# Kernel tuning notes

Hardware: AMD Instinct MI355X
Metric: run time of the kernel (lower is better)

The kernel has to match this reference:

```python
import jax, jax.numpy as jnp
import numpy as np

B, T, C = 4, 4096, 1024
HEAD_SIZE = 64
HEAD_OUT = 64


def setup_inputs() -> dict:
    key = jax.random.key(0)
    kx, kk, kq, kv = jax.random.split(key, 4)
    x = jax.random.normal(kx, (B, T, C), dtype=jnp.float32)
    # nn.Linear(in, out, bias=False): weight [out, in]; y = x @ W.T
    Wk = jax.random.normal(kk, (HEAD_SIZE, C), dtype=jnp.float32) * (C ** -0.5)
    Wq = jax.random.normal(kq, (HEAD_SIZE, C), dtype=jnp.float32) * (C ** -0.5)
    Wv = jax.random.normal(kv, (HEAD_OUT, C), dtype=jnp.float32) * (C ** -0.5)
    return {"x": x, "Wk": Wk, "Wq": Wq, "Wv": Wv}


def reference(x, Wk, Wq, Wv):
    Tlen = x.shape[1]
    k = jnp.einsum('btc,hc->bth', x, Wk)  # [B,T,Hs]
    q = jnp.einsum('btc,hc->bth', x, Wq)  # [B,T,Hs]
    v = jnp.einsum('btc,oc->bto', x, Wv)  # [B,T,Ho]
    scale = HEAD_SIZE ** -0.5
    scores = jnp.einsum('bih,bjh->bij', q, k) * scale  # [B,T,T]
    # torch.tril(ones, diagonal=1): allowed where j <= i+1 (note: one superdiagonal kept)
    i = jnp.arange(Tlen)[:, None]
    j = jnp.arange(Tlen)[None, :]
    allowed = j <= i + 1
    masked = jnp.where(allowed, scores, -jnp.inf)
    # NOTE: original scales AGAIN inside softmax (double scaling, faithful)
    weights = jax.nn.softmax(masked * scale, axis=-1)
    return jnp.einsum('bij,bjo->bio', weights, v)  # [B,T,Ho]
```

## Files before the change

### kernel.cpp

```cpp
#include <hip/hip_runtime.h>

#define BB 4
#define TT 4096
#define CC 1024
#define HH 64
#define AW 8

typedef unsigned short us;
typedef us v8u __attribute__((ext_vector_type(8)));
typedef us v4u __attribute__((ext_vector_type(4)));
typedef __bf16 v8bf __attribute__((ext_vector_type(8)));
typedef float v4f __attribute__((ext_vector_type(4)));

__device__ __forceinline__ us f2bf(float f) {
  return __builtin_bit_cast(us, (__bf16)f);
}
__device__ __forceinline__ v8bf ldb(const us* p) {
  return __builtin_bit_cast(v8bf, *(const v8u*)p);
}

__global__ __launch_bounds__(256) void convertw_kernel(const float* __restrict__ Wk,
                                                       const float* __restrict__ Wq,
                                                       const float* __restrict__ Wv,
                                                       us* __restrict__ wpack) {
  const int g = blockIdx.x * 256 + threadIdx.x;
  const int t = g >> 13;
  const int rem = g & 8191;
  const int oc = rem >> 11;
  const int kc = (rem >> 6) & 31;
  const int lane = rem & 63;
  const float* W = (t == 0) ? Wq : ((t == 1) ? Wk : Wv);
  const int h  = oc * 16 + (lane & 15);
  const int d0 = kc * 32 + (lane >> 4) * 8;
  const float4* src = (const float4*)(W + h * CC + d0);
  const float4 f0 = src[0], f1 = src[1];
  v8u o;
  o[0]=f2bf(f0.x); o[1]=f2bf(f0.y); o[2]=f2bf(f0.z); o[3]=f2bf(f0.w);
  o[4]=f2bf(f1.x); o[5]=f2bf(f1.y); o[6]=f2bf(f1.z); o[7]=f2bf(f1.w);
  *(v8u*)(wpack + (size_t)g * 8) = o;
}


__global__ __launch_bounds__(768, 6) void proj_kernel(
    const float* __restrict__ x, const us* __restrict__ wpack,
    us* __restrict__ qpack, us* __restrict__ kpack, us* __restrict__ vpack)
{
  __shared__ __align__(16) us xlds[32][1048];

  const int tid  = threadIdx.x;
  const int lane = tid & 63, w = tid >> 6;
  const int i16 = lane & 15, quad = lane >> 4;
  const int t = w >> 2, oc = w & 3;
  const int rows0 = blockIdx.x * 32;

  const float4* xg4 = (const float4*)(x + (size_t)rows0 * CC);
  for (int i = tid; i < 8192; i += 768) {
    const float4 f = xg4[i];
    v4u o; o[0]=f2bf(f.x); o[1]=f2bf(f.y); o[2]=f2bf(f.z); o[3]=f2bf(f.w);
    *(v4u*)&xlds[i >> 8][(i & 255) * 4] = o;
  }
  __syncthreads();

  const us* wp = wpack + (size_t)w * 16384 + lane * 8;
  v4f zero = {0.f, 0.f, 0.f, 0.f};
  v4f acc[2] = {zero, zero};

  #pragma unroll 4
  for (int kc = 0; kc < 32; kc++) {
    const v8bf wf = ldb(wp + kc * 512);
    #pragma unroll
    for (int rg = 0; rg < 2; rg++) {
      const v8bf a = ldb(&xlds[rg * 16 + i16][kc * 32 + quad * 8]);
      acc[rg] = __builtin_amdgcn_mfma_f32_16x16x32_bf16(a, wf, acc[rg], 0, 0, 0);
    }
  }

  const float COEF = 0.015625f * 1.4426950408889634f;
  const int b    = rows0 >> 12;
  const int tile = (rows0 & (TT - 1)) >> 5;

  if (t < 2) {
    us* dst = t ? kpack : qpack;
    const float c = t ? 1.0f : COEF;
    const int h = oc * 16 + i16;
    #pragma unroll
    for (int rg = 0; rg < 2; rg++) {
      #pragma unroll
      for (int r = 0; r < 4; r++) {
        const int tr = quad * 4 + r;
        const int lane2 = tr + 16 * ((h >> 3) & 3);
        const size_t idx = ((((size_t)(b * 128 + tile) * 2 + rg) * 2 + (h >> 5)) * 64 + lane2) * 8 + (h & 7);
        dst[idx] = f2bf(acc[rg][r] * c);
      }
    }
  } else {
    #pragma unroll
    for (int rg = 0; rg < 2; rg++) {
      const int lane3 = i16 + 16 * (rg * 2 + (quad >> 1));
      v4u pk;
      #pragma unroll
      for (int r = 0; r < 4; r++) pk[r] = f2bf(acc[rg][r]);
      *(v4u*)&vpack[(((size_t)(b * 128 + tile) * 4 + oc) * 64 + lane3) * 8 + (quad & 1) * 4] = pk;
    }
  }
}

__global__ __launch_bounds__(512, 4) void attn_kernel(
    const us* __restrict__ qpack, const us* __restrict__ kpack,
    const us* __restrict__ vpack, float* __restrict__ out)
{
  __shared__ float shbuf[AW][2148];

  const int tid  = threadIdx.x;
  const int lane = tid & 63, warp = tid >> 6;
  const int i16 = lane & 15, quad = lane >> 4;

  const int p = blockIdx.x & 255, s = blockIdx.x >> 8;
  const int b  = p & 3;
  const int q0 = p >> 2;
  const int qb = s ? (127 - q0) : q0;
  const int i0 = qb << 5;
  const int nt = min(qb + 2, 128);

  us* Pw = (us*)shbuf[warp];
  const float NEGINF = -__builtin_inff();

  v8bf qf[2][2];
  #pragma unroll
  for (int ih = 0; ih < 2; ih++)
    #pragma unroll
    for (int g = 0; g < 2; g++)
      qf[ih][g] = ldb(qpack + ((((size_t)(b * 128 + qb) * 2 + ih) * 2 + g) * 64 + lane) * 8);

  v4f zero = {0.f, 0.f, 0.f, 0.f};
  v4f oacc[2][4];
  #pragma unroll
  for (int ih = 0; ih < 2; ih++)
    #pragma unroll
    for (int oc = 0; oc < 4; oc++) oacc[ih][oc] = zero;
  float lsum[2] = {0.f, 0.f};

  auto loadK = [&](int t, v8bf kf[2][2]) {
    #pragma unroll
    for (int f = 0; f < 2; f++)
      #pragma unroll
      for (int g = 0; g < 2; g++)
        kf[f][g] = ldb(kpack + ((((size_t)(b * 128 + t) * 2 + f) * 2 + g) * 64 + lane) * 8);
  };
  auto loadV = [&](int t, v8bf vf[4]) {
    #pragma unroll
    for (int oc = 0; oc < 4; oc++)
      vf[oc] = ldb(vpack + (((size_t)(b * 128 + t) * 4 + oc) * 64 + lane) * 8);
  };
  auto qk_exp_store = [&](int t, const v8bf kf[2][2], int buf) {
    v4f sacc[2][2];
    #pragma unroll
    for (int ih = 0; ih < 2; ih++)
      #pragma unroll
      for (int f = 0; f < 2; f++) {
        v4f sv = zero;
        sv = __builtin_amdgcn_mfma_f32_16x16x32_bf16(kf[f][0], qf[ih][0], sv, 0, 0, 0);
        sv = __builtin_amdgcn_mfma_f32_16x16x32_bf16(kf[f][1], qf[ih][1], sv, 0, 0, 0);
        sacc[ih][f] = sv;
      }
    const int j0 = t * 32;
    const bool needMask = (t >= qb);
    #pragma unroll
    for (int ih = 0; ih < 2; ih++) {
      float ps[8];
      #pragma unroll
      for (int f = 0; f < 2; f++)
        #pragma unroll
        for (int r = 0; r < 4; r++) {
          float sv = fminf(sacc[ih][f][r], 80.f);
          if (needMask) {
            const int j = j0 + f * 16 + quad * 4 + r;
            const int i = i0 + ih * 16 + i16;
            sv = (j <= i + 1) ? sv : NEGINF;
          }
          ps[f * 4 + r] = exp2f(sv);
        }
      {
        const float s0 = ps[0] + ps[1], s1 = ps[2] + ps[3];
        const float s2 = ps[4] + ps[5], s3 = ps[6] + ps[7];
        lsum[ih] += (s0 + s1) + (s2 + s3);
      }
      #pragma unroll
      for (int f = 0; f < 2; f++) {
        v4u pk;
        #pragma unroll
        for (int r = 0; r < 4; r++) pk[r] = f2bf(ps[f * 4 + r]);
        *(v4u*)&Pw[buf * 1280 + ih * 640 + i16 * 40 + f * 16 + quad * 4] = pk;
      }
    }
  };
  auto pv = [&](int buf, const v8bf vf[4]) {
    #pragma unroll
    for (int ih = 0; ih < 2; ih++) {
      v8bf pf = __builtin_bit_cast(v8bf, *(const v8u*)&Pw[buf * 1280 + ih * 640 + i16 * 40 + quad * 8]);
      #pragma unroll
      for (int oc = 0; oc < 4; oc++)
        oacc[ih][oc] = __builtin_amdgcn_mfma_f32_16x16x32_bf16(vf[oc], pf, oacc[ih][oc], 0, 0, 0);
    }
  };

  int t = warp, buf = 0;
  if (t < nt) {
    v8bf kcur[2][2], knxt[2][2], vprev[4];
    loadK(t, kcur); loadV(t, vprev);
    if (t + AW < nt) loadK(t + AW, knxt);
    qk_exp_store(t, kcur, 0);
    #pragma unroll 2
    for (t += AW; t < nt; t += AW) {
      pv(buf, vprev);
      loadV(t, vprev);
      #pragma unroll
      for (int f = 0; f < 2; f++)
        #pragma unroll
        for (int g = 0; g < 2; g++) kcur[f][g] = knxt[f][g];
      if (t + AW < nt) loadK(t + AW, knxt);
      qk_exp_store(t, kcur, buf ^ 1);
      buf ^= 1;
    }
    pv(buf, vprev);
  }

  #pragma unroll
  for (int ih = 0; ih < 2; ih++) {
    lsum[ih] += __shfl_xor(lsum[ih], 16, 64);
    lsum[ih] += __shfl_xor(lsum[ih], 32, 64);
    #pragma unroll
    for (int oc = 0; oc < 4; oc++)
      #pragma unroll
      for (int r = 0; r < 4; r++)
        shbuf[warp][(oc * 16 + quad * 4 + r) * 33 + ih * 16 + i16] = oacc[ih][oc][r];
  }
  if (lane < 16) {
    shbuf[warp][2112 + lane]      = lsum[0];
    shbuf[warp][2112 + 16 + lane] = lsum[1];
  }
  __syncthreads();

  const int o  = tid & 63;
  const int iw = tid >> 6;
  #pragma unroll
  for (int rr = 0; rr < 4; rr++) {
    const int i = iw + rr * 8;
    float L = 0.f, O = 0.f;
    #pragma unroll
    for (int w = 0; w < AW; w++) {
      L += shbuf[w][2112 + i];
      O += shbuf[w][o * 33 + i];
    }
    out[(size_t)(b * TT + i0 + i) * HH + o] = O / L;
  }
}

extern "C" void kernel_launch(void* const* d_in, const int* in_sizes, int n_in,
                              void* d_out, int out_size, void* d_ws, size_t ws_size,
                              hipStream_t stream) {
  const size_t NWP = 3 * 4 * 32 * 64 * 8;
  const size_t NP  = (size_t)BB * TT * HH;

  us* wpack = (us*)d_ws;
  us* qpack = wpack + NWP;
  us* kpack = qpack + NP;
  us* vpack = kpack + NP;
  float* out = (float*)d_out;

  convertw_kernel<<<96, 256, 0, stream>>>(
      (const float*)d_in[1], (const float*)d_in[2], (const float*)d_in[3], wpack);
  proj_kernel<<<BB * TT / 32, 768, 0, stream>>>(
      (const float*)d_in[0], wpack, qpack, kpack, vpack);
  attn_kernel<<<512, 512, 0, stream>>>(qpack, kpack, vpack, out);
}
```

Measured before the change: 129.1 us.

## Split projection K-dimension into two halves to overlap x loads with MFMA

```diff
diff --git a/kernel.cpp b/kernel.cpp
--- a/kernel.cpp
+++ b/kernel.cpp
@@ -45,7 +45,7 @@
     const float* __restrict__ x, const us* __restrict__ wpack,
     us* __restrict__ qpack, us* __restrict__ kpack, us* __restrict__ vpack)
 {
-  __shared__ __align__(16) us xlds[32][1048];
+  __shared__ __align__(16) us xlds[2][32][524];
 
   const int tid  = threadIdx.x;
   const int lane = tid & 63, w = tid >> 6;
@@ -54,23 +54,56 @@
   const int rows0 = blockIdx.x * 32;
 
   const float4* xg4 = (const float4*)(x + (size_t)rows0 * CC);
-  for (int i = tid; i < 8192; i += 768) {
-    const float4 f = xg4[i];
-    v4u o; o[0]=f2bf(f.x); o[1]=f2bf(f.y); o[2]=f2bf(f.z); o[3]=f2bf(f.w);
-    *(v4u*)&xlds[i >> 8][(i & 255) * 4] = o;
+
+  #pragma unroll
+  for (int j = 0; j < 6; j++) {
+    const int i = tid + j * 768;
+    if (i < 4096) {
+      const int r = i >> 7, c = i & 127;
+      const float4 f = xg4[r * 256 + c];
+      v4u o; o[0]=f2bf(f.x); o[1]=f2bf(f.y); o[2]=f2bf(f.z); o[3]=f2bf(f.w);
+      *(v4u*)&xlds[0][r][c * 4] = o;
+    }
   }
   __syncthreads();
+
+  float4 fB[6];
+  #pragma unroll
+  for (int j = 0; j < 6; j++) {
+    const int i = tid + j * 768;
+    if (i < 4096) fB[j] = xg4[(i >> 7) * 256 + 128 + (i & 127)];
+  }
 
   const us* wp = wpack + (size_t)w * 16384 + lane * 8;
   v4f zero = {0.f, 0.f, 0.f, 0.f};
   v4f acc[2] = {zero, zero};
 
   #pragma unroll 4
-  for (int kc = 0; kc < 32; kc++) {
+  for (int kc = 0; kc < 16; kc++) {
     const v8bf wf = ldb(wp + kc * 512);
     #pragma unroll
     for (int rg = 0; rg < 2; rg++) {
-      const v8bf a = ldb(&xlds[rg * 16 + i16][kc * 32 + quad * 8]);
+      const v8bf a = ldb(&xlds[0][rg * 16 + i16][kc * 32 + quad * 8]);
+      acc[rg] = __builtin_amdgcn_mfma_f32_16x16x32_bf16(a, wf, acc[rg], 0, 0, 0);
+    }
+  }
+
+  #pragma unroll
+  for (int j = 0; j < 6; j++) {
+    const int i = tid + j * 768;
+    if (i < 4096) {
+      v4u o; o[0]=f2bf(fB[j].x); o[1]=f2bf(fB[j].y); o[2]=f2bf(fB[j].z); o[3]=f2bf(fB[j].w);
+      *(v4u*)&xlds[1][i >> 7][(i & 127) * 4] = o;
+    }
+  }
+  __syncthreads();
+
+  #pragma unroll 4
+  for (int kc = 16; kc < 32; kc++) {
+    const v8bf wf = ldb(wp + kc * 512);
+    #pragma unroll
+    for (int rg = 0; rg < 2; rg++) {
+      const v8bf a = ldb(&xlds[1][rg * 16 + i16][(kc - 16) * 32 + quad * 8]);
       acc[rg] = __builtin_amdgcn_mfma_f32_16x16x32_bf16(a, wf, acc[rg], 0, 0, 0);
     }
   }
```

New measurement: 161.9 us. 1.25x slower.
